# Performance work log

Measured on AMD Instinct MI355X. Metric: run time of the kernel, lower is better.

## Reference

```python
import jax, jax.numpy as jnp
import numpy as np

BS, NMEM, NQ, D, H, NL = 16, 256, 63, 512, 512, 1
INI = 0.01

def setup_inputs() -> dict:
    key = jax.random.key(0)
    ks = jax.random.split(key, 13)
    s_ih = 1.0 / np.sqrt(H)
    return {
        "knowledge_state": jax.random.normal(ks[0], (BS, NMEM, D), jnp.float32),
        "knowledge_num": jax.random.randint(ks[1], (BS,), 1, NMEM),
        "lstm_in": jax.random.normal(ks[2], (BS, NQ, D), jnp.float32),
        "init_h": jax.random.uniform(ks[3], (NL, H), jnp.float32, -INI, INI),
        "init_c": jax.random.uniform(ks[4], (NL, H), jnp.float32, -INI, INI),
        "init_i": jax.random.uniform(ks[5], (D,), jnp.float32, -0.1, 0.1),
        "w_ih": jax.random.uniform(ks[6], (4 * H, D), jnp.float32, -s_ih, s_ih),
        "w_hh": jax.random.uniform(ks[7], (4 * H, H), jnp.float32, -s_ih, s_ih),
        "b_ih": jax.random.uniform(ks[8], (4 * H,), jnp.float32, -s_ih, s_ih),
        "b_hh": jax.random.uniform(ks[9], (4 * H,), jnp.float32, -s_ih, s_ih),
        "attn_wm": jax.random.normal(ks[10], (D, H), jnp.float32) * np.sqrt(2.0 / (D + H)),
        "attn_wq": jax.random.normal(ks[11], (H, H), jnp.float32) * np.sqrt(2.0 / (H + H)),
        "attn_v": jax.random.uniform(ks[12], (H,), jnp.float32, -INI, INI),
    }


def _lstm(x_tbd, h0, c0, w_ih, w_hh, b_ih, b_hh):
    # x_tbd: [T, bs, D]; single-layer LSTM, PyTorch gate order (i, f, g, o)
    b = b_ih + b_hh

    def step(carry, x_t):
        h, c = carry
        gates = x_t @ w_ih.T + h @ w_hh.T + b  # [bs, 4H]
        i, f, g, o = jnp.split(gates, 4, axis=-1)
        c = jax.nn.sigmoid(f) * c + jax.nn.sigmoid(i) * jnp.tanh(g)
        h = jax.nn.sigmoid(o) * jnp.tanh(c)
        return (h, c), h

    _, ys = jax.lax.scan(step, (h0, c0), x_tbd)
    return ys  # [T, bs, H]


def reference(knowledge_state, knowledge_num, lstm_in, init_h, init_c, init_i,
              w_ih, w_hh, b_ih, b_hh, attn_wm, attn_wq, attn_v):
    bs = knowledge_state.shape[0]
    # _prepare: project memory, broadcast init states
    attn_feat = jnp.einsum('bmd,dh->bmh', knowledge_state, attn_wm)  # [bs, n_mem, H]
    # prepend learned init input token, go seq-first for the LSTM
    x = jnp.concatenate(
        [jnp.broadcast_to(init_i[None, None, :], (bs, 1, init_i.shape[0])), lstm_in],
        axis=1)                                   # [bs, T, D], T = n_q + 1
    x = jnp.swapaxes(x, 0, 1)                     # [T, bs, D]
    h0 = jnp.broadcast_to(init_h[0][None, :], (bs, init_h.shape[1]))
    c0 = jnp.broadcast_to(init_c[0][None, :], (bs, init_c.shape[1]))
    ys = _lstm(x, h0, c0, w_ih, w_hh, b_ih, b_hh)  # [T, bs, H]
    query = jnp.swapaxes(ys, 0, 1)                 # [bs, T, H]
    # additive (Bahdanau) attention score
    q = jnp.einsum('bth,hk->btk', query, attn_wq)  # [bs, T, H]
    s = jnp.tanh(attn_feat[:, None, :, :] + q[:, :, None, :])  # [bs, T, n_mem, H]
    score = jnp.einsum('btmh,h->btm', s, attn_v)   # [bs, T, n_mem]
    return score
```

## Files before the change

kernel.cpp:

```cpp
#include <hip/hip_runtime.h>

#define BS   16
#define NMEM 256
#define NQ   63
#define T    64
#define D    512
#define H    512
#define G4   2048

#define K2C  2.885390081777927f

typedef __attribute__((ext_vector_type(8))) short short8;
typedef __attribute__((ext_vector_type(4))) float float4v;

enum : size_t {
    OFF_XW  = 0,
    OFF_YS  = OFF_XW  + (size_t)T*BS*G4,
    OFF_HB  = OFF_YS  + (size_t)(T+1)*BS*H,
    OFF_AF  = OFF_HB  + (size_t)(T+1)*BS*H,
    OFF_Q   = OFF_AF  + (size_t)BS*NMEM*H,
    OFF_X   = OFF_Q   + (size_t)T*BS*H,
    OFF_B   = OFF_X   + (size_t)T*BS*D,
    OFF_BAR = OFF_B   + (size_t)G4,
};

__device__ inline unsigned short bf16_rn(float x) {
    union { float f; unsigned u; } a; a.f = x;
    unsigned r = a.u + 0x7FFFu + ((a.u >> 16) & 1u);
    return (unsigned short)(r >> 16);
}
__device__ inline float bf16_to_f(unsigned short s) {
    union { float f; unsigned u; } a; a.u = ((unsigned)s) << 16;
    return a.f;
}

__global__ void prep(const float* __restrict__ lstm_in, const float* __restrict__ init_h,
                     const float* __restrict__ init_i,
                     const float* __restrict__ b_ih, const float* __restrict__ b_hh,
                     float* __restrict__ xbuf, float* __restrict__ biasbuf,
                     unsigned short* __restrict__ hb0)
{
    int i = blockIdx.x * blockDim.x + threadIdx.x;
    const int NX = T*BS*D;
    if (i < NX) {
        int d = i & 511; int r = i >> 9; int t = r >> 4; int b = r & 15;
        float v = (t == 0) ? init_i[d] : lstm_in[((size_t)(b*NQ) + (t-1))*D + d];
        __builtin_nontemporal_store(v, xbuf + i);
    } else if (i < NX + G4) {
        int j = i - NX; biasbuf[j] = b_ih[j] + b_hh[j];
    } else if (i < NX + G4 + 8192) {
        int e = i - (NX + G4);
        int iw = e & 7;
        int k = ((e >> 3) >> 4) * 8 + iw;
        float h0 = init_h[k];
        unsigned short hi = bf16_rn(h0);
        unsigned short lo = bf16_rn(h0 - bf16_to_f(hi));
        hb0[e] = hi;
        hb0[8192 + e] = lo;
    }
}

template<bool BT>
__device__ inline void gemm_unit(const float* __restrict__ A, const float* __restrict__ B,
                                 float* __restrict__ C, const float* __restrict__ bias,
                                 int N, int K, int tm, int tn, int t2)
{
    const int w = t2 >> 6, lane = t2 & 63;
    const int quad = lane >> 4, l15 = lane & 15;
    const int am = tm + w*16 + l15;
    float4v acch[4] = {{0,0,0,0},{0,0,0,0},{0,0,0,0},{0,0,0,0}};
    float4v accl[4] = {{0,0,0,0},{0,0,0,0},{0,0,0,0},{0,0,0,0}};
    for (int k0 = 0; k0 < K; k0 += 32) {
        const float* ap = A + (size_t)am*K + k0 + quad*8;
        float4 a0 = *(const float4*)ap, a1 = *(const float4*)(ap+4);
        float av[8] = {a0.x,a0.y,a0.z,a0.w,a1.x,a1.y,a1.z,a1.w};
        short8 ah, al;
#pragma unroll
        for (int i = 0; i < 8; ++i) {
            unsigned short hi = bf16_rn(av[i]);
            ah[i] = (short)hi; al[i] = (short)bf16_rn(av[i] - bf16_to_f(hi));
        }
#pragma unroll
        for (int ni = 0; ni < 4; ++ni) {
            const int n = tn + ni*16 + l15;
            float bv[8];
            if (BT) {
                const float* bp = B + (size_t)n*K + k0 + quad*8;
                float4 b0 = *(const float4*)bp, b1 = *(const float4*)(bp+4);
                bv[0]=b0.x; bv[1]=b0.y; bv[2]=b0.z; bv[3]=b0.w;
                bv[4]=b1.x; bv[5]=b1.y; bv[6]=b1.z; bv[7]=b1.w;
            } else {
                const float* bp = B + (size_t)(k0 + quad*8)*N + n;
#pragma unroll
                for (int i = 0; i < 8; ++i) bv[i] = bp[(size_t)i*N];
            }
            short8 bh, bl;
#pragma unroll
            for (int i = 0; i < 8; ++i) {
                unsigned short hi = bf16_rn(bv[i]);
                bh[i] = (short)hi; bl[i] = (short)bf16_rn(bv[i] - bf16_to_f(hi));
            }
            acch[ni] = __builtin_amdgcn_mfma_f32_16x16x32_bf16(ah, bh, acch[ni], 0, 0, 0);
            accl[ni] = __builtin_amdgcn_mfma_f32_16x16x32_bf16(al, bh, accl[ni], 0, 0, 0);
            accl[ni] = __builtin_amdgcn_mfma_f32_16x16x32_bf16(ah, bl, accl[ni], 0, 0, 0);
        }
    }
#pragma unroll
    for (int ni = 0; ni < 4; ++ni) {
        const int n = tn + ni*16 + l15;
        float bb = bias ? bias[n] : 0.f;
        float4v r = acch[ni] + accl[ni];
#pragma unroll
        for (int j = 0; j < 4; ++j) {
            int row = tm + w*16 + quad*4 + j;
            __builtin_nontemporal_store(r[j] + bb, C + (size_t)row*N + n);
        }
    }
}

template<bool BT>
__global__ __launch_bounds__(256) void gemm_mfma(const float* __restrict__ A,
                                                 const float* __restrict__ B,
                                                 float* __restrict__ C,
                                                 const float* __restrict__ bias,
                                                 int N, int K)
{
    gemm_unit<BT>(A, B, C, bias, N, K, blockIdx.y*64, blockIdx.x*64, threadIdx.x);
}

__global__ __launch_bounds__(512, 2) void lstm_af(
    const float* __restrict__ xW,
    const float* __restrict__ w_hh,
    const float* __restrict__ init_c,
    const float* __restrict__ ks,
    const float* __restrict__ wm,
    float* __restrict__ ys,
    unsigned short* __restrict__ hbuf,
    float* __restrict__ af,
    int* __restrict__ flags)
{
    const int tid = threadIdx.x;

    if (blockIdx.x >= 32) {
        const int u = tid >> 8;
        const int tau = (blockIdx.x - 32)*2 + u;
        gemm_unit<false>(ks, wm, af, nullptr, H, D, (tau >> 3)*64, (tau & 7)*64, tid & 255);
        return;
    }

    __shared__ float smem[3328];
    float* part = smem;
    float* cst  = smem + 2048;
    float* xwb  = smem + 2304;

    const int jt    = blockIdx.x;
    const int w     = tid >> 6;
    const int g     = w >> 1;
    const int khalf = w & 1;
    const int lane  = tid & 63;
    const int quad  = lane >> 4;
    const int l15   = lane & 15;

    short8 bh[8], bl[8];
    {
        const int row = g*512 + jt*16 + l15;
        const float* wr = w_hh + (size_t)row*H + khalf*256 + quad*8;
#pragma unroll
        for (int kt = 0; kt < 8; ++kt) {
            const float* wp = wr + kt*32;
#pragma unroll
            for (int i = 0; i < 8; ++i) {
                float v = wp[i];
                unsigned short hi = bf16_rn(v);
                bh[kt][i] = (short)hi;
                bl[kt][i] = (short)bf16_rn(v - bf16_to_f(hi));
            }
        }
    }

    const int b2 = tid >> 4, j16 = tid & 15;
    if (tid < 256) cst[b2*16 + j16] = init_c[jt*16 + j16];
    if (tid >= 256) {
        int ti = tid - 256;
        int bb = ti >> 4, s = ti & 15;
        int gg = s & 3, j4 = (s >> 2) << 2;
        float4 v = *(const float4*)(xW + (size_t)bb*G4 + gg*512 + jt*16 + j4);
        float* dst = xwb + gg*256 + bb*16 + j4;
        dst[0]=v.x; dst[1]=v.y; dst[2]=v.z; dst[3]=v.w;
    }
    __syncthreads();

    for (int t = 0; t < T; ++t) {
        const short8* hhi = (const short8*)(hbuf + (size_t)t*16384);
        const short8* hlo = hhi + 1024;
        short8 ah[8], al[8];
#pragma unroll
        for (int kt = 0; kt < 8; ++kt) {
            int c = ((khalf*8 + kt)*4 + quad)*16 + l15;
            ah[kt] = hhi[c];
            al[kt] = hlo[c];
        }
        float4v a0 = {0.f,0.f,0.f,0.f}, a1 = {0.f,0.f,0.f,0.f};
#pragma unroll
        for (int kt = 0; kt < 8; ++kt) {
            a0 = __builtin_amdgcn_mfma_f32_16x16x32_bf16(ah[kt], bh[kt], a0, 0, 0, 0);
            a1 = __builtin_amdgcn_mfma_f32_16x16x32_bf16(al[kt], bh[kt], a1, 0, 0, 0);
            a1 = __builtin_amdgcn_mfma_f32_16x16x32_bf16(ah[kt], bl[kt], a1, 0, 0, 0);
        }
        a0 += a1;
        *(float4v*)&part[(w*64 + lane)*4] = a0;
        __syncthreads();

        if (tid < 256) {
            const int lsrc = ((b2 >> 2)*16 + j16)*4, r = b2 & 3;
            float gi = part[(0*256) + lsrc + r] + part[(1*256) + lsrc + r] + xwb[0*256 + b2*16 + j16];
            float gf = part[(2*256) + lsrc + r] + part[(3*256) + lsrc + r] + xwb[1*256 + b2*16 + j16];
            float gg = part[(4*256) + lsrc + r] + part[(5*256) + lsrc + r] + xwb[2*256 + b2*16 + j16];
            float go = part[(6*256) + lsrc + r] + part[(7*256) + lsrc + r] + xwb[3*256 + b2*16 + j16];
            float si = 1.f/(1.f+__expf(-gi));
            float sf = 1.f/(1.f+__expf(-gf));
            float so = 1.f/(1.f+__expf(-go));
            float cn = sf*cst[b2*16 + j16] + si*tanhf(gg);
            float hn = so*tanhf(cn);
            cst[b2*16 + j16] = cn;
            __builtin_nontemporal_store(hn, ys + (size_t)(t+1)*BS*H + b2*H + jt*16 + j16);
            const int k = jt*16 + j16;
            const int e = ((k >> 3)*16 + b2)*8 + (k & 7);
            unsigned short hi = bf16_rn(hn);
            unsigned short* hb1 = hbuf + (size_t)(t+1)*16384;
            hb1[e]        = hi;
            hb1[8192 + e] = bf16_rn(hn - bf16_to_f(hi));
        }
        __syncthreads();

        if (t < T-1) {
            if (tid == 0)
                __hip_atomic_store(&flags[jt*16], t+1, __ATOMIC_RELEASE, __HIP_MEMORY_SCOPE_AGENT);
            if (tid >= 256) {
                int ti = tid - 256;
                int bb = ti >> 4, s = ti & 15;
                int gg2 = s & 3, j4 = (s >> 2) << 2;
                float4 v = *(const float4*)(xW + (size_t)(t+1)*BS*G4 + bb*G4 + gg2*512 + jt*16 + j4);
                float* dst = xwb + gg2*256 + bb*16 + j4;
                dst[0]=v.x; dst[1]=v.y; dst[2]=v.z; dst[3]=v.w;
            }
            if (tid < 64) {
                const int fidx = (tid & 31) << 4;
                int v;
                do {
                    v = __hip_atomic_load(&flags[fidx], __ATOMIC_RELAXED, __HIP_MEMORY_SCOPE_AGENT);
                } while (!__all(v >= t+1));
                __builtin_amdgcn_fence(__ATOMIC_ACQUIRE, "agent");
            }
            __syncthreads();
        }
    }
}

__global__ __launch_bounds__(256) void attn(const float* __restrict__ af,
                                            const float* __restrict__ q,
                                            const float* __restrict__ v,
                                            float* __restrict__ out)
{
    __shared__ float afs[64][68];
    __shared__ float qs[4][516];
    __shared__ float vs[512];
    const int tid = threadIdx.x;
    const int mc = blockIdx.x, tc = blockIdx.y, b = blockIdx.z;
    for (int i = tid; i < 4*128; i += 256) {
        int t = i >> 7, h4 = (i & 127) << 2;
        float4 x = *(const float4*)(q + ((size_t)((tc*4 + t)*16 + b) << 9) + h4);
        x.x *= K2C; x.y *= K2C; x.z *= K2C; x.w *= K2C;
        *(float4*)&qs[t][h4] = x;
    }
    for (int i = tid; i < 128; i += 256)
        *(float4*)&vs[i << 2] = *(const float4*)(v + (i << 2));
    const int ml = tid & 63, tg = tid >> 6;
    float acc = 0.f;
    for (int hc = 0; hc < 8; ++hc) {
        __syncthreads();
        for (int i = tid; i < 64*16; i += 256) {
            int m = i >> 4, h4 = (i & 15) << 2;
            float4 x = *(const float4*)(af + ((size_t)(b*NMEM + mc*64 + m) << 9) + hc*64 + h4);
            x.x *= K2C; x.y *= K2C; x.z *= K2C; x.w *= K2C;
            *(float4*)&afs[m][h4] = x;
        }
        __syncthreads();
#pragma unroll
        for (int h8 = 0; h8 < 8; ++h8) {
            float4 a0 = *(const float4*)&afs[ml][h8*8 + 0];
            float4 a1 = *(const float4*)&afs[ml][h8*8 + 4];
            float4 v0 = *(const float4*)&vs[hc*64 + h8*8 + 0];
            float4 v1 = *(const float4*)&vs[hc*64 + h8*8 + 4];
            float4 q0 = *(const float4*)&qs[tg][hc*64 + h8*8 + 0];
            float4 q1 = *(const float4*)&qs[tg][hc*64 + h8*8 + 4];
            const float* ap0 = (const float*)&a0; const float* ap1 = (const float*)&a1;
            const float* vp0 = (const float*)&v0; const float* vp1 = (const float*)&v1;
            const float* qp0 = (const float*)&q0; const float* qp1 = (const float*)&q1;
            float s = acc;
#pragma unroll
            for (int j = 0; j < 4; ++j) {
                float e = exp2f(ap0[j] + qp0[j]);
                s = fmaf(vp0[j], __builtin_amdgcn_rcpf(e + 1.f), s);
            }
#pragma unroll
            for (int j = 0; j < 4; ++j) {
                float e = exp2f(ap1[j] + qp1[j]);
                s = fmaf(vp1[j], __builtin_amdgcn_rcpf(e + 1.f), s);
            }
            acc = s;
        }
    }
    float Sv = 0.f;
    for (int i = 0; i < 512; i += 4) {
        float4 t4 = *(const float4*)&vs[i];
        Sv += t4.x + t4.y + t4.z + t4.w;
    }
    out[((size_t)b*T + tc*4 + tg)*NMEM + mc*64 + ml] = Sv - 2.f*acc;
}

extern "C" void kernel_launch(void* const* d_in, const int* in_sizes, int n_in,
                              void* d_out, int out_size, void* d_ws, size_t ws_size,
                              hipStream_t stream)
{
    const float* ks      = (const float*)d_in[0];
    const float* lstm_in = (const float*)d_in[2];
    const float* init_h  = (const float*)d_in[3];
    const float* init_c  = (const float*)d_in[4];
    const float* init_i  = (const float*)d_in[5];
    const float* w_ih    = (const float*)d_in[6];
    const float* w_hh    = (const float*)d_in[7];
    const float* b_ih    = (const float*)d_in[8];
    const float* b_hh    = (const float*)d_in[9];
    const float* wm      = (const float*)d_in[10];
    const float* wq      = (const float*)d_in[11];
    const float* av      = (const float*)d_in[12];

    float* ws   = (float*)d_ws;
    float* xW   = ws + OFF_XW;
    float* ys   = ws + OFF_YS;
    unsigned short* hbuf = (unsigned short*)(ws + OFF_HB);
    float* af   = ws + OFF_AF;
    float* qb   = ws + OFF_Q;
    float* xb   = ws + OFF_X;
    float* bias = ws + OFF_B;
    int*   flags= (int*)(ws + OFF_BAR);

    hipMemsetAsync(flags, 0, 512*sizeof(int), stream);

    const int prep_n = T*BS*D + G4 + 8192;
    prep<<<(prep_n + 255)/256, 256, 0, stream>>>(lstm_in, init_h, init_i,
                                                 b_ih, b_hh, xb, bias, hbuf);
    gemm_mfma<true><<<dim3(32, 16), 256, 0, stream>>>(xb, w_ih, xW, bias, G4, D);
    lstm_af<<<288, 512, 0, stream>>>(xW, w_hh, init_c, ks, wm, ys, hbuf, af, flags);
    gemm_mfma<false><<<dim3(8, 16), 256, 0, stream>>>(ys + BS*H, wq, qb, nullptr, H, H);
    attn<<<dim3(4, 16, 16), 256, 0, stream>>>(af, qb, av, (float*)d_out);
}
```

Measured before the change: 464.4 us.

## Fuse input-projection GEMM into persistent LSTM kernel with per-timestep readiness counters

Removes the separate x·W_ih GEMM launch. Worker blocks in the persistent LSTM kernel compute those tiles and publish per-row-tile completion counters, and the recurrent blocks wait only for the timestep group they need, so the projection overlaps with the serial recurrence. The bf16 hi/lo halves of h are packed into one 32-bit word so a single atomic store publishes both, and readers use 64-bit atomic loads and unpack them. Spin loops now call s_sleep. The cost is extra atomic traffic and lost nontemporal stores, and recurrent blocks may stall early if the projection tiles finish slowly.

```diff
diff --git a/kernel.cpp b/kernel.cpp
--- a/kernel.cpp
+++ b/kernel.cpp
@@ -38,7 +38,7 @@
                      const float* __restrict__ init_i,
                      const float* __restrict__ b_ih, const float* __restrict__ b_hh,
                      float* __restrict__ xbuf, float* __restrict__ biasbuf,
-                     unsigned short* __restrict__ hb0)
+                     unsigned* __restrict__ hb0)
 {
     int i = blockIdx.x * blockDim.x + threadIdx.x;
     const int NX = T*BS*D;
@@ -53,14 +53,13 @@
         int iw = e & 7;
         int k = ((e >> 3) >> 4) * 8 + iw;
         float h0 = init_h[k];
-        unsigned short hi = bf16_rn(h0);
-        unsigned short lo = bf16_rn(h0 - bf16_to_f(hi));
-        hb0[e] = hi;
-        hb0[8192 + e] = lo;
-    }
-}
-
-template<bool BT>
+        unsigned hi = bf16_rn(h0);
+        unsigned lo = bf16_rn(h0 - bf16_to_f((unsigned short)hi));
+        hb0[e] = hi | (lo << 16);
+    }
+}
+
+template<bool BT, bool AT>
 __device__ inline void gemm_unit(const float* __restrict__ A, const float* __restrict__ B,
                                  float* __restrict__ C, const float* __restrict__ bias,
                                  int N, int K, int tm, int tn, int t2)
@@ -113,7 +112,12 @@
 #pragma unroll
         for (int j = 0; j < 4; ++j) {
             int row = tm + w*16 + quad*4 + j;
-            __builtin_nontemporal_store(r[j] + bb, C + (size_t)row*N + n);
+            float val = r[j] + bb;
+            if (AT)
+                __hip_atomic_store(C + (size_t)row*N + n, val,
+                                   __ATOMIC_RELAXED, __HIP_MEMORY_SCOPE_AGENT);
+            else
+                __builtin_nontemporal_store(val, C + (size_t)row*N + n);
         }
     }
 }
@@ -125,26 +129,41 @@
                                                  const float* __restrict__ bias,
                                                  int N, int K)
 {
-    gemm_unit<BT>(A, B, C, bias, N, K, blockIdx.y*64, blockIdx.x*64, threadIdx.x);
-}
-
-__global__ __launch_bounds__(512, 2) void lstm_af(
-    const float* __restrict__ xW,
+    gemm_unit<BT, false>(A, B, C, bias, N, K, blockIdx.y*64, blockIdx.x*64, threadIdx.x);
+}
+
+__global__ __launch_bounds__(512, 2) void mega(
+    float* __restrict__ xW,
     const float* __restrict__ w_hh,
     const float* __restrict__ init_c,
     const float* __restrict__ ks,
     const float* __restrict__ wm,
+    const float* __restrict__ xb,
+    const float* __restrict__ w_ih,
+    const float* __restrict__ bias,
     float* __restrict__ ys,
-    unsigned short* __restrict__ hbuf,
+    unsigned* __restrict__ hbuf,
     float* __restrict__ af,
     int* __restrict__ flags)
 {
     const int tid = threadIdx.x;
+    int* hflag = flags;
+    int* xcnt  = flags + 512;
 
     if (blockIdx.x >= 32) {
-        const int u = tid >> 8;
-        const int tau = (blockIdx.x - 32)*2 + u;
-        gemm_unit<false>(ks, wm, af, nullptr, H, D, (tau >> 3)*64, (tau & 7)*64, tid & 255);
+        const int u  = (blockIdx.x - 32)*2 + (tid >> 8);
+        const int t2 = tid & 255;
+        for (int tau = u; tau < 512; tau += 448) {
+            const int mt = tau >> 5, ntt = tau & 31;
+            gemm_unit<true, true>(xb, w_ih, xW, bias, G4, D, mt*64, ntt*64, t2);
+            __syncthreads();
+            if (t2 == 0)
+                __hip_atomic_fetch_add(&xcnt[mt*16], 1, __ATOMIC_RELEASE, __HIP_MEMORY_SCOPE_AGENT);
+        }
+        for (int tau = u; tau < 512; tau += 448) {
+            const int mt = tau >> 3, ntt = tau & 7;
+            gemm_unit<false, true>(ks, wm, af, nullptr, H, D, mt*64, ntt*64, t2);
+        }
         return;
     }
 
@@ -181,6 +200,8 @@
     const int b2 = tid >> 4, j16 = tid & 15;
     if (tid < 256) cst[b2*16 + j16] = init_c[jt*16 + j16];
     if (tid >= 256) {
+        while (__hip_atomic_load(&xcnt[0], __ATOMIC_RELAXED, __HIP_MEMORY_SCOPE_AGENT) < 32)
+            __builtin_amdgcn_s_sleep(1);
         int ti = tid - 256;
         int bb = ti >> 4, s = ti & 15;
         int gg = s & 3, j4 = (s >> 2) << 2;
@@ -190,15 +211,29 @@
     }
     __syncthreads();
 
+    union U8 { unsigned u[4]; short8 s; };
+
     for (int t = 0; t < T; ++t) {
-        const short8* hhi = (const short8*)(hbuf + (size_t)t*16384);
-        const short8* hlo = hhi + 1024;
+        const unsigned long long* hp = (const unsigned long long*)(hbuf + (size_t)t*8192);
         short8 ah[8], al[8];
 #pragma unroll
         for (int kt = 0; kt < 8; ++kt) {
-            int c = ((khalf*8 + kt)*4 + quad)*16 + l15;
-            ah[kt] = hhi[c];
-            al[kt] = hlo[c];
+            const int base = ((((khalf*8 + kt)*4 + quad)*16 + l15) << 2);
+            unsigned long long q0 = __hip_atomic_load(hp + base + 0, __ATOMIC_RELAXED, __HIP_MEMORY_SCOPE_AGENT);
+            unsigned long long q1 = __hip_atomic_load(hp + base + 1, __ATOMIC_RELAXED, __HIP_MEMORY_SCOPE_AGENT);
+            unsigned long long q2 = __hip_atomic_load(hp + base + 2, __ATOMIC_RELAXED, __HIP_MEMORY_SCOPE_AGENT);
+            unsigned long long q3 = __hip_atomic_load(hp + base + 3, __ATOMIC_RELAXED, __HIP_MEMORY_SCOPE_AGENT);
+            U8 Ah, Al;
+            unsigned u0, u1;
+            u0 = (unsigned)q0; u1 = (unsigned)(q0 >> 32);
+            Ah.u[0] = (u0 & 0xffffu) | (u1 << 16);  Al.u[0] = (u0 >> 16) | (u1 & 0xffff0000u);
+            u0 = (unsigned)q1; u1 = (unsigned)(q1 >> 32);
+            Ah.u[1] = (u0 & 0xffffu) | (u1 << 16);  Al.u[1] = (u0 >> 16) | (u1 & 0xffff0000u);
+            u0 = (unsigned)q2; u1 = (unsigned)(q2 >> 32);
+            Ah.u[2] = (u0 & 0xffffu) | (u1 << 16);  Al.u[2] = (u0 >> 16) | (u1 & 0xffff0000u);
+            u0 = (unsigned)q3; u1 = (unsigned)(q3 >> 32);
+            Ah.u[3] = (u0 & 0xffffu) | (u1 << 16);  Al.u[3] = (u0 >> 16) | (u1 & 0xffff0000u);
+            ah[kt] = Ah.s; al[kt] = Al.s;
         }
         float4v a0 = {0.f,0.f,0.f,0.f}, a1 = {0.f,0.f,0.f,0.f};
 #pragma unroll
@@ -223,20 +258,24 @@
             float cn = sf*cst[b2*16 + j16] + si*tanhf(gg);
             float hn = so*tanhf(cn);
             cst[b2*16 + j16] = cn;
-            __builtin_nontemporal_store(hn, ys + (size_t)(t+1)*BS*H + b2*H + jt*16 + j16);
+            __hip_atomic_store(ys + (size_t)(t+1)*BS*H + b2*H + jt*16 + j16, hn,
+                               __ATOMIC_RELAXED, __HIP_MEMORY_SCOPE_AGENT);
             const int k = jt*16 + j16;
             const int e = ((k >> 3)*16 + b2)*8 + (k & 7);
-            unsigned short hi = bf16_rn(hn);
-            unsigned short* hb1 = hbuf + (size_t)(t+1)*16384;
-            hb1[e]        = hi;
-            hb1[8192 + e] = bf16_rn(hn - bf16_to_f(hi));
+            unsigned hi = bf16_rn(hn);
+            unsigned lo = bf16_rn(hn - bf16_to_f((unsigned short)hi));
+            __hip_atomic_store(hbuf + (size_t)(t+1)*8192 + e, hi | (lo << 16),
+                               __ATOMIC_RELAXED, __HIP_MEMORY_SCOPE_AGENT);
         }
         __syncthreads();
 
         if (t < T-1) {
             if (tid == 0)
-                __hip_atomic_store(&flags[jt*16], t+1, __ATOMIC_RELEASE, __HIP_MEMORY_SCOPE_AGENT);
+                __hip_atomic_store(&hflag[jt*16], t+1, __ATOMIC_RELEASE, __HIP_MEMORY_SCOPE_AGENT);
             if (tid >= 256) {
+                const int grp = ((t+1) >> 2) * 16;
+                while (__hip_atomic_load(&xcnt[grp], __ATOMIC_RELAXED, __HIP_MEMORY_SCOPE_AGENT) < 32)
+                    __builtin_amdgcn_s_sleep(1);
                 int ti = tid - 256;
                 int bb = ti >> 4, s = ti & 15;
                 int gg2 = s & 3, j4 = (s >> 2) << 2;
@@ -246,11 +285,11 @@
             }
             if (tid < 64) {
                 const int fidx = (tid & 31) << 4;
-                int v;
-                do {
-                    v = __hip_atomic_load(&flags[fidx], __ATOMIC_RELAXED, __HIP_MEMORY_SCOPE_AGENT);
-                } while (!__all(v >= t+1));
-                __builtin_amdgcn_fence(__ATOMIC_ACQUIRE, "agent");
+                for (;;) {
+                    int v = __hip_atomic_load(&hflag[fidx], __ATOMIC_RELAXED, __HIP_MEMORY_SCOPE_AGENT);
+                    if (__all(v >= t+1)) break;
+                    __builtin_amdgcn_s_sleep(1);
+                }
             }
             __syncthreads();
         }
@@ -339,20 +378,20 @@
     float* ws   = (float*)d_ws;
     float* xW   = ws + OFF_XW;
     float* ys   = ws + OFF_YS;
-    unsigned short* hbuf = (unsigned short*)(ws + OFF_HB);
+    unsigned* hbuf = (unsigned*)(ws + OFF_HB);
     float* af   = ws + OFF_AF;
     float* qb   = ws + OFF_Q;
     float* xb   = ws + OFF_X;
     float* bias = ws + OFF_B;
     int*   flags= (int*)(ws + OFF_BAR);
 
-    hipMemsetAsync(flags, 0, 512*sizeof(int), stream);
+    hipMemsetAsync(flags, 0, 1024*sizeof(int), stream);
 
     const int prep_n = T*BS*D + G4 + 8192;
     prep<<<(prep_n + 255)/256, 256, 0, stream>>>(lstm_in, init_h, init_i,
                                                  b_ih, b_hh, xb, bias, hbuf);
-    gemm_mfma<true><<<dim3(32, 16), 256, 0, stream>>>(xb, w_ih, xW, bias, G4, D);
-    lstm_af<<<288, 512, 0, stream>>>(xW, w_hh, init_c, ks, wm, ys, hbuf, af, flags);
+    mega<<<256, 512, 0, stream>>>(xW, w_hh, init_c, ks, wm, xb, w_ih, bias,
+                                  ys, hbuf, af, flags);
     gemm_mfma<false><<<dim3(8, 16), 256, 0, stream>>>(ys + BS*H, wq, qb, nullptr, H, H);
     attn<<<dim3(4, 16, 16), 256, 0, stream>>>(af, qb, av, (float*)d_out);
 }
```

Measured after the change: 512.5 us. 1.1x slower.

## Fuse all stages into one persistent kernel with flag-based inter-stage dataflow

Applied to the files above, without the earlier changes.

Replaces the five separate launches (prep, input GEMM, LSTM+memory projection, query GEMM, attention) with a single persistent kernel. 32 blocks run the recurrent LSTM while the other 224 blocks compute the input projection, the memory projection, the query projection and the attention tiles. These worker blocks are coordinated by atomic counters, so later stages can start on finished timesteps while the recurrence is still running. The prep pass is removed: the input concat, bias sum and initial-hidden bf16 split are computed on the fly. This removes launch gaps and extra passes over memory, at the cost of spin-waits, lower occupancy (launch bounds 512,1) and the LSTM blocks now depending on producers being scheduled concurrently.

```diff
diff --git a/kernel.cpp b/kernel.cpp
--- a/kernel.cpp
+++ b/kernel.cpp
@@ -19,9 +19,7 @@
     OFF_HB  = OFF_YS  + (size_t)(T+1)*BS*H,
     OFF_AF  = OFF_HB  + (size_t)(T+1)*BS*H,
     OFF_Q   = OFF_AF  + (size_t)BS*NMEM*H,
-    OFF_X   = OFF_Q   + (size_t)T*BS*H,
-    OFF_B   = OFF_X   + (size_t)T*BS*D,
-    OFF_BAR = OFF_B   + (size_t)G4,
+    OFF_BAR = OFF_Q   + (size_t)T*BS*H,
 };
 
 __device__ inline unsigned short bf16_rn(float x) {
@@ -34,44 +32,27 @@
     return a.f;
 }
 
-__global__ void prep(const float* __restrict__ lstm_in, const float* __restrict__ init_h,
-                     const float* __restrict__ init_i,
-                     const float* __restrict__ b_ih, const float* __restrict__ b_hh,
-                     float* __restrict__ xbuf, float* __restrict__ biasbuf,
-                     unsigned short* __restrict__ hb0)
-{
-    int i = blockIdx.x * blockDim.x + threadIdx.x;
-    const int NX = T*BS*D;
-    if (i < NX) {
-        int d = i & 511; int r = i >> 9; int t = r >> 4; int b = r & 15;
-        float v = (t == 0) ? init_i[d] : lstm_in[((size_t)(b*NQ) + (t-1))*D + d];
-        __builtin_nontemporal_store(v, xbuf + i);
-    } else if (i < NX + G4) {
-        int j = i - NX; biasbuf[j] = b_ih[j] + b_hh[j];
-    } else if (i < NX + G4 + 8192) {
-        int e = i - (NX + G4);
-        int iw = e & 7;
-        int k = ((e >> 3) >> 4) * 8 + iw;
-        float h0 = init_h[k];
-        unsigned short hi = bf16_rn(h0);
-        unsigned short lo = bf16_rn(h0 - bf16_to_f(hi));
-        hb0[e] = hi;
-        hb0[8192 + e] = lo;
-    }
-}
-
-template<bool BT>
+template<int MODE>
 __device__ inline void gemm_unit(const float* __restrict__ A, const float* __restrict__ B,
-                                 float* __restrict__ C, const float* __restrict__ bias,
+                                 float* __restrict__ C,
+                                 const float* __restrict__ bias1, const float* __restrict__ bias2,
+                                 const float* __restrict__ init_i,
                                  int N, int K, int tm, int tn, int t2)
 {
     const int w = t2 >> 6, lane = t2 & 63;
     const int quad = lane >> 4, l15 = lane & 15;
     const int am = tm + w*16 + l15;
+    const float* arow;
+    if (MODE == 1) {
+        const int tt = am >> 4, bb = am & 15;
+        arow = (tt == 0) ? init_i : (A + ((size_t)bb*NQ + (tt-1))*D);
+    } else {
+        arow = A + (size_t)am*K;
+    }
     float4v acch[4] = {{0,0,0,0},{0,0,0,0},{0,0,0,0},{0,0,0,0}};
     float4v accl[4] = {{0,0,0,0},{0,0,0,0},{0,0,0,0},{0,0,0,0}};
     for (int k0 = 0; k0 < K; k0 += 32) {
-        const float* ap = A + (size_t)am*K + k0 + quad*8;
+        const float* ap = arow + k0 + quad*8;
         float4 a0 = *(const float4*)ap, a1 = *(const float4*)(ap+4);
         float av[8] = {a0.x,a0.y,a0.z,a0.w,a1.x,a1.y,a1.z,a1.w};
         short8 ah, al;
@@ -84,7 +65,7 @@
         for (int ni = 0; ni < 4; ++ni) {
             const int n = tn + ni*16 + l15;
             float bv[8];
-            if (BT) {
+            if (MODE == 1) {
                 const float* bp = B + (size_t)n*K + k0 + quad*8;
                 float4 b0 = *(const float4*)bp, b1 = *(const float4*)(bp+4);
                 bv[0]=b0.x; bv[1]=b0.y; bv[2]=b0.z; bv[3]=b0.w;
@@ -108,7 +89,7 @@
 #pragma unroll
     for (int ni = 0; ni < 4; ++ni) {
         const int n = tn + ni*16 + l15;
-        float bb = bias ? bias[n] : 0.f;
+        float bb = (MODE == 1) ? (bias1[n] + bias2[n]) : 0.f;
         float4v r = acch[ni] + accl[ni];
 #pragma unroll
         for (int j = 0; j < 4; ++j) {
@@ -118,37 +99,139 @@
     }
 }
 
-template<bool BT>
-__global__ __launch_bounds__(256) void gemm_mfma(const float* __restrict__ A,
-                                                 const float* __restrict__ B,
-                                                 float* __restrict__ C,
-                                                 const float* __restrict__ bias,
-                                                 int N, int K)
+__device__ inline void attn_unit(const float* __restrict__ af, const float* __restrict__ q,
+                                 const float* __restrict__ v, float* __restrict__ out,
+                                 int mc, int tc, int b, int t2, float* lds)
 {
-    gemm_unit<BT>(A, B, C, bias, N, K, blockIdx.y*64, blockIdx.x*64, threadIdx.x);
-}
-
-__global__ __launch_bounds__(512, 2) void lstm_af(
-    const float* __restrict__ xW,
+    float* afs = lds;
+    float* qs  = lds + 4352;
+    float* vs  = lds + 6416;
+    __syncthreads();
+    for (int i = t2; i < 4*128; i += 256) {
+        int t = i >> 7, h4 = (i & 127) << 2;
+        float4 x = *(const float4*)(q + ((size_t)((tc*4 + t)*16 + b) << 9) + h4);
+        x.x *= K2C; x.y *= K2C; x.z *= K2C; x.w *= K2C;
+        *(float4*)&qs[t*516 + h4] = x;
+    }
+    for (int i = t2; i < 128; i += 256)
+        *(float4*)&vs[i << 2] = *(const float4*)(v + (i << 2));
+    const int ml = t2 & 63, tg = t2 >> 6;
+    float acc = 0.f;
+    for (int hc = 0; hc < 8; ++hc) {
+        __syncthreads();
+        for (int i = t2; i < 64*16; i += 256) {
+            int m = i >> 4, h4 = (i & 15) << 2;
+            float4 x = *(const float4*)(af + ((size_t)(b*NMEM + mc*64 + m) << 9) + hc*64 + h4);
+            x.x *= K2C; x.y *= K2C; x.z *= K2C; x.w *= K2C;
+            *(float4*)&afs[m*68 + h4] = x;
+        }
+        __syncthreads();
+#pragma unroll
+        for (int h8 = 0; h8 < 8; ++h8) {
+            float4 a0 = *(const float4*)&afs[ml*68 + h8*8 + 0];
+            float4 a1 = *(const float4*)&afs[ml*68 + h8*8 + 4];
+            float4 v0 = *(const float4*)&vs[hc*64 + h8*8 + 0];
+            float4 v1 = *(const float4*)&vs[hc*64 + h8*8 + 4];
+            float4 q0 = *(const float4*)&qs[tg*516 + hc*64 + h8*8 + 0];
+            float4 q1 = *(const float4*)&qs[tg*516 + hc*64 + h8*8 + 4];
+            const float* ap0 = (const float*)&a0; const float* ap1 = (const float*)&a1;
+            const float* vp0 = (const float*)&v0; const float* vp1 = (const float*)&v1;
+            const float* qp0 = (const float*)&q0; const float* qp1 = (const float*)&q1;
+            float s = acc;
+#pragma unroll
+            for (int j = 0; j < 4; ++j) {
+                float e = exp2f(ap0[j] + qp0[j]);
+                s = fmaf(vp0[j], __builtin_amdgcn_rcpf(e + 1.f), s);
+            }
+#pragma unroll
+            for (int j = 0; j < 4; ++j) {
+                float e = exp2f(ap1[j] + qp1[j]);
+                s = fmaf(vp1[j], __builtin_amdgcn_rcpf(e + 1.f), s);
+            }
+            acc = s;
+        }
+    }
+    float Sv = 0.f;
+    for (int i = 0; i < 512; i += 4) {
+        float4 t4 = *(const float4*)&vs[i];
+        Sv += t4.x + t4.y + t4.z + t4.w;
+    }
+    out[((size_t)b*T + tc*4 + tg)*NMEM + mc*64 + ml] = Sv - 2.f*acc;
+}
+
+__global__ __launch_bounds__(512, 1) void mega(
+    const float* __restrict__ lstm_in,
+    const float* __restrict__ init_h,
+    const float* __restrict__ init_c,
+    const float* __restrict__ init_i,
+    const float* __restrict__ w_ih,
     const float* __restrict__ w_hh,
-    const float* __restrict__ init_c,
+    const float* __restrict__ b_ih,
+    const float* __restrict__ b_hh,
     const float* __restrict__ ks,
     const float* __restrict__ wm,
-    float* __restrict__ ys,
-    unsigned short* __restrict__ hbuf,
-    float* __restrict__ af,
+    const float* __restrict__ wq,
+    const float* __restrict__ av,
+    float* __restrict__ xW, float* __restrict__ ys,
+    unsigned short* __restrict__ hbuf, float* __restrict__ af,
+    float* __restrict__ qb, float* __restrict__ out,
     int* __restrict__ flags)
 {
+    __shared__ float smem[13856];
     const int tid = threadIdx.x;
+    int* hflag = flags;
+    int* xcnt  = flags + 512;
+    int* qbcnt = flags + 768;
+    int* afcnt = flags + 1024;
 
     if (blockIdx.x >= 32) {
-        const int u = tid >> 8;
-        const int tau = (blockIdx.x - 32)*2 + u;
-        gemm_unit<false>(ks, wm, af, nullptr, H, D, (tau >> 3)*64, (tau & 7)*64, tid & 255);
+        const int uu = tid >> 8;
+        const int u  = (blockIdx.x - 32)*2 + uu;
+        const int t2 = tid & 255;
+        const int lane = tid & 63;
+        for (int tau = u; tau < 512; tau += 448) {
+            const int mt = tau >> 5, nt_ = tau & 31;
+            gemm_unit<1>(lstm_in, w_ih, xW, b_ih, b_hh, init_i, G4, D, mt*64, nt_*64, t2);
+            __syncthreads();
+            if (t2 == 0)
+                __hip_atomic_fetch_add(&xcnt[mt*16], 1, __ATOMIC_RELEASE, __HIP_MEMORY_SCOPE_AGENT);
+        }
+        for (int tau = u; tau < 512; tau += 448) {
+            gemm_unit<0>(ks, wm, af, nullptr, nullptr, nullptr, H, D, (tau>>3)*64, (tau&7)*64, t2);
+            __syncthreads();
+            if (t2 == 0)
+                __hip_atomic_fetch_add(&afcnt[0], 1, __ATOMIC_RELEASE, __HIP_MEMORY_SCOPE_AGENT);
+        }
+        if (u < 128) {
+            const int mt = u >> 3, nt_ = u & 7;
+            const int need = mt*4 + 4;
+            const int fidx = (lane & 31) << 4;
+            for (;;) {
+                int v = __hip_atomic_load(&hflag[fidx], __ATOMIC_RELAXED, __HIP_MEMORY_SCOPE_AGENT);
+                if (__all(v >= need)) break;
+                __builtin_amdgcn_s_sleep(32);
+            }
+            __builtin_amdgcn_fence(__ATOMIC_ACQUIRE, "agent");
+            gemm_unit<2>(ys + BS*H, wq, qb, nullptr, nullptr, nullptr, H, H, mt*64, nt_*64, t2);
+        }
+        __syncthreads();
+        if (u < 128 && t2 == 0)
+            __hip_atomic_fetch_add(&qbcnt[(u>>3)*16], 1, __ATOMIC_RELEASE, __HIP_MEMORY_SCOPE_AGENT);
+        float* myLds = smem + uu*6928;
+        for (int tau = u; tau < 1024; tau += 448) {
+            const int tc = tau >> 6, mc = (tau >> 4) & 3, bb = tau & 15;
+            for (;;) {
+                int v1 = __hip_atomic_load(&qbcnt[tc*16], __ATOMIC_RELAXED, __HIP_MEMORY_SCOPE_AGENT);
+                int v2 = __hip_atomic_load(&afcnt[0], __ATOMIC_RELAXED, __HIP_MEMORY_SCOPE_AGENT);
+                if (v1 >= 8 && v2 >= 512) break;
+                __builtin_amdgcn_s_sleep(32);
+            }
+            __builtin_amdgcn_fence(__ATOMIC_ACQUIRE, "agent");
+            attn_unit(af, qb, av, out, mc, tc, bb, t2, myLds);
+        }
         return;
     }
 
-    __shared__ float smem[3328];
     float* part = smem;
     float* cst  = smem + 2048;
     float* xwb  = smem + 2304;
@@ -181,6 +264,9 @@
     const int b2 = tid >> 4, j16 = tid & 15;
     if (tid < 256) cst[b2*16 + j16] = init_c[jt*16 + j16];
     if (tid >= 256) {
+        while (__hip_atomic_load(&xcnt[0], __ATOMIC_RELAXED, __HIP_MEMORY_SCOPE_AGENT) < 32)
+            __builtin_amdgcn_s_sleep(1);
+        __builtin_amdgcn_fence(__ATOMIC_ACQUIRE, "agent");
         int ti = tid - 256;
         int bb = ti >> 4, s = ti & 15;
         int gg = s & 3, j4 = (s >> 2) << 2;
@@ -191,14 +277,30 @@
     __syncthreads();
 
     for (int t = 0; t < T; ++t) {
-        const short8* hhi = (const short8*)(hbuf + (size_t)t*16384);
-        const short8* hlo = hhi + 1024;
         short8 ah[8], al[8];
-#pragma unroll
-        for (int kt = 0; kt < 8; ++kt) {
-            int c = ((khalf*8 + kt)*4 + quad)*16 + l15;
-            ah[kt] = hhi[c];
-            al[kt] = hlo[c];
+        if (t == 0) {
+#pragma unroll
+            for (int kt = 0; kt < 8; ++kt) {
+                const int kbase = ((khalf*8 + kt)*4 + quad)*8;
+                float4 h0a = *(const float4*)(init_h + kbase);
+                float4 h0b = *(const float4*)(init_h + kbase + 4);
+                float hv[8] = {h0a.x,h0a.y,h0a.z,h0a.w,h0b.x,h0b.y,h0b.z,h0b.w};
+#pragma unroll
+                for (int i = 0; i < 8; ++i) {
+                    unsigned short hi = bf16_rn(hv[i]);
+                    ah[kt][i] = (short)hi;
+                    al[kt][i] = (short)bf16_rn(hv[i] - bf16_to_f(hi));
+                }
+            }
+        } else {
+            const short8* hhi = (const short8*)(hbuf + (size_t)t*16384);
+            const short8* hlo = hhi + 1024;
+#pragma unroll
+            for (int kt = 0; kt < 8; ++kt) {
+                int c = ((khalf*8 + kt)*4 + quad)*16 + l15;
+                ah[kt] = hhi[c];
+                al[kt] = hlo[c];
+            }
         }
         float4v a0 = {0.f,0.f,0.f,0.f}, a1 = {0.f,0.f,0.f,0.f};
 #pragma unroll
@@ -223,7 +325,8 @@
             float cn = sf*cst[b2*16 + j16] + si*tanhf(gg);
             float hn = so*tanhf(cn);
             cst[b2*16 + j16] = cn;
-            __builtin_nontemporal_store(hn, ys + (size_t)(t+1)*BS*H + b2*H + jt*16 + j16);
+            __hip_atomic_store(ys + (size_t)(t+1)*BS*H + b2*H + jt*16 + j16, hn,
+                               __ATOMIC_RELAXED, __HIP_MEMORY_SCOPE_AGENT);
             const int k = jt*16 + j16;
             const int e = ((k >> 3)*16 + b2)*8 + (k & 7);
             unsigned short hi = bf16_rn(hn);
@@ -235,8 +338,12 @@
 
         if (t < T-1) {
             if (tid == 0)
-                __hip_atomic_store(&flags[jt*16], t+1, __ATOMIC_RELEASE, __HIP_MEMORY_SCOPE_AGENT);
+                __hip_atomic_store(&hflag[jt*16], t+1, __ATOMIC_RELEASE, __HIP_MEMORY_SCOPE_AGENT);
             if (tid >= 256) {
+                const int grp = ((t+1) >> 2) * 16;
+                while (__hip_atomic_load(&xcnt[grp], __ATOMIC_RELAXED, __HIP_MEMORY_SCOPE_AGENT) < 32)
+                    __builtin_amdgcn_s_sleep(1);
+                __builtin_amdgcn_fence(__ATOMIC_ACQUIRE, "agent");
                 int ti = tid - 256;
                 int bb = ti >> 4, s = ti & 15;
                 int gg2 = s & 3, j4 = (s >> 2) << 2;
@@ -246,77 +353,18 @@
             }
             if (tid < 64) {
                 const int fidx = (tid & 31) << 4;
-                int v;
-                do {
-                    v = __hip_atomic_load(&flags[fidx], __ATOMIC_RELAXED, __HIP_MEMORY_SCOPE_AGENT);
-                } while (!__all(v >= t+1));
+                for (;;) {
+                    int v = __hip_atomic_load(&hflag[fidx], __ATOMIC_RELAXED, __HIP_MEMORY_SCOPE_AGENT);
+                    if (__all(v >= t+1)) break;
+                    __builtin_amdgcn_s_sleep(1);
+                }
                 __builtin_amdgcn_fence(__ATOMIC_ACQUIRE, "agent");
             }
             __syncthreads();
         }
     }
-}
-
-__global__ __launch_bounds__(256) void attn(const float* __restrict__ af,
-                                            const float* __restrict__ q,
-                                            const float* __restrict__ v,
-                                            float* __restrict__ out)
-{
-    __shared__ float afs[64][68];
-    __shared__ float qs[4][516];
-    __shared__ float vs[512];
-    const int tid = threadIdx.x;
-    const int mc = blockIdx.x, tc = blockIdx.y, b = blockIdx.z;
-    for (int i = tid; i < 4*128; i += 256) {
-        int t = i >> 7, h4 = (i & 127) << 2;
-        float4 x = *(const float4*)(q + ((size_t)((tc*4 + t)*16 + b) << 9) + h4);
-        x.x *= K2C; x.y *= K2C; x.z *= K2C; x.w *= K2C;
-        *(float4*)&qs[t][h4] = x;
-    }
-    for (int i = tid; i < 128; i += 256)
-        *(float4*)&vs[i << 2] = *(const float4*)(v + (i << 2));
-    const int ml = tid & 63, tg = tid >> 6;
-    float acc = 0.f;
-    for (int hc = 0; hc < 8; ++hc) {
-        __syncthreads();
-        for (int i = tid; i < 64*16; i += 256) {
-            int m = i >> 4, h4 = (i & 15) << 2;
-            float4 x = *(const float4*)(af + ((size_t)(b*NMEM + mc*64 + m) << 9) + hc*64 + h4);
-            x.x *= K2C; x.y *= K2C; x.z *= K2C; x.w *= K2C;
-            *(float4*)&afs[m][h4] = x;
-        }
-        __syncthreads();
-#pragma unroll
-        for (int h8 = 0; h8 < 8; ++h8) {
-            float4 a0 = *(const float4*)&afs[ml][h8*8 + 0];
-            float4 a1 = *(const float4*)&afs[ml][h8*8 + 4];
-            float4 v0 = *(const float4*)&vs[hc*64 + h8*8 + 0];
-            float4 v1 = *(const float4*)&vs[hc*64 + h8*8 + 4];
-            float4 q0 = *(const float4*)&qs[tg][hc*64 + h8*8 + 0];
-            float4 q1 = *(const float4*)&qs[tg][hc*64 + h8*8 + 4];
-            const float* ap0 = (const float*)&a0; const float* ap1 = (const float*)&a1;
-            const float* vp0 = (const float*)&v0; const float* vp1 = (const float*)&v1;
-            const float* qp0 = (const float*)&q0; const float* qp1 = (const float*)&q1;
-            float s = acc;
-#pragma unroll
-            for (int j = 0; j < 4; ++j) {
-                float e = exp2f(ap0[j] + qp0[j]);
-                s = fmaf(vp0[j], __builtin_amdgcn_rcpf(e + 1.f), s);
-            }
-#pragma unroll
-            for (int j = 0; j < 4; ++j) {
-                float e = exp2f(ap1[j] + qp1[j]);
-                s = fmaf(vp1[j], __builtin_amdgcn_rcpf(e + 1.f), s);
-            }
-            acc = s;
-        }
-    }
-    float Sv = 0.f;
-    for (int i = 0; i < 512; i += 4) {
-        float4 t4 = *(const float4*)&vs[i];
-        Sv += t4.x + t4.y + t4.z + t4.w;
-    }
-    out[((size_t)b*T + tc*4 + tg)*NMEM + mc*64 + ml] = Sv - 2.f*acc;
+    if (tid == 0)
+        __hip_atomic_store(&hflag[jt*16], T, __ATOMIC_RELEASE, __HIP_MEMORY_SCOPE_AGENT);
 }
 
 extern "C" void kernel_launch(void* const* d_in, const int* in_sizes, int n_in,
@@ -342,17 +390,10 @@
     unsigned short* hbuf = (unsigned short*)(ws + OFF_HB);
     float* af   = ws + OFF_AF;
     float* qb   = ws + OFF_Q;
-    float* xb   = ws + OFF_X;
-    float* bias = ws + OFF_B;
     int*   flags= (int*)(ws + OFF_BAR);
 
-    hipMemsetAsync(flags, 0, 512*sizeof(int), stream);
-
-    const int prep_n = T*BS*D + G4 + 8192;
-    prep<<<(prep_n + 255)/256, 256, 0, stream>>>(lstm_in, init_h, init_i,
-                                                 b_ih, b_hh, xb, bias, hbuf);
-    gemm_mfma<true><<<dim3(32, 16), 256, 0, stream>>>(xb, w_ih, xW, bias, G4, D);
-    lstm_af<<<288, 512, 0, stream>>>(xW, w_hh, init_c, ks, wm, ys, hbuf, af, flags);
-    gemm_mfma<false><<<dim3(8, 16), 256, 0, stream>>>(ys + BS*H, wq, qb, nullptr, H, H);
-    attn<<<dim3(4, 16, 16), 256, 0, stream>>>(af, qb, av, (float*)d_out);
-}
+    hipMemsetAsync(flags, 0, 2048*sizeof(int), stream);
+    mega<<<256, 512, 0, stream>>>(lstm_in, init_h, init_c, init_i,
+                                  w_ih, w_hh, b_ih, b_hh, ks, wm, wq, av,
+                                  xW, ys, hbuf, af, qb, (float*)d_out, flags);
+}
```

Result: slower. 576.1 us (+24.1%).
